# Kernel optimization log

Measured on AMD Instinct MI355X. Metric: run time of the kernel, lower is better.

## Reference

```python
import jax, jax.numpy as jnp
import numpy as np

VOCAB, D_EMB, Z_DIM, HID = 32000, 512, 256, 1024
B, T = 32, 128
PAD_IDX = 0

def setup_inputs() -> dict:
    key = jax.random.key(0)
    ks = jax.random.split(key, 12)
    s_emb = 1.0  # nn.Embedding default N(0,1)
    u = lambda k, shape, fan: jax.random.uniform(k, shape, jnp.float32, -1.0, 1.0) / np.sqrt(fan)
    emb = jax.random.normal(ks[0], (VOCAB, D_EMB), jnp.float32) * s_emb
    emb = emb.at[PAD_IDX].set(0.0)  # padding_idx row zeroed
    inp = {
        "z": jax.random.normal(ks[1], (B, Z_DIM), jnp.float32),
        "x": jax.random.randint(ks[2], (B, T), 0, VOCAB, jnp.int32),
        "W_h": u(ks[3], (HID, Z_DIM), Z_DIM),
        "b_h": u(ks[4], (HID,), Z_DIM),
        "emb": emb,
        "W_ih": u(ks[5], (4 * HID, D_EMB), HID),
        "W_hh": u(ks[6], (4 * HID, HID), HID),
        "b_ih": u(ks[7], (4 * HID,), HID),
        "b_hh": u(ks[8], (4 * HID,), HID),
        "W_out": u(ks[9], (VOCAB, HID), HID),
        "b_out": u(ks[10], (VOCAB,), HID),
    }
    return inp

def _lstm_decode(z, x, W_h, b_h, emb, W_ih, W_hh, b_ih, b_hh, W_out, b_out):
    h0 = jnp.tanh(z @ W_h.T + b_h)            # [B, H]
    c0 = jnp.zeros_like(h0)
    e = emb[x]                                 # [B, T, D]
    # Precompute input-side gate projections for all timesteps at once.
    x_gates = jnp.einsum('btd,gd->btg', e, W_ih) + b_ih + b_hh  # [B, T, 4H]
    x_gates_t = jnp.swapaxes(x_gates, 0, 1)    # [T, B, 4H]

    def step(carry, xg_t):
        h, c = carry
        gates = xg_t + h @ W_hh.T              # [B, 4H]
        i, f, g, o = jnp.split(gates, 4, axis=-1)  # torch gate order i,f,g,o
        i, f, o = jax.nn.sigmoid(i), jax.nn.sigmoid(f), jax.nn.sigmoid(o)
        g = jnp.tanh(g)
        c = f * c + i * g
        h = o * jnp.tanh(c)
        return (h, c), h

    _, hs = jax.lax.scan(step, (h0, c0), x_gates_t)  # hs: [T, B, H]
    out = jnp.swapaxes(hs, 0, 1)               # [B, T, H]
    return jnp.einsum('bth,vh->btv', out, W_out) + b_out  # [B, T, V]

def reference(z, x, W_h, b_h, emb, W_ih, W_hh, b_ih, b_hh, W_out, b_out):
    return _lstm_decode(z, x, W_h, b_h, emb, W_ih, W_hh, b_ih, b_hh, W_out, b_out)
```

## Files before the change

kernel.cpp:

```cpp
#include <hip/hip_runtime.h>

typedef _Float16 f16;
typedef _Float16 f16x8 __attribute__((ext_vector_type(8)));
typedef _Float16 f16x4 __attribute__((ext_vector_type(4)));
typedef float    f32x4 __attribute__((ext_vector_type(4)));
typedef unsigned long long ull;

static constexpr int Bb  = 32;
static constexpr int Tt  = 128;
static constexpr int HID = 1024;
static constexpr int ZD  = 256;
static constexpr int DE  = 512;
static constexpr int VOC = 32000;
static constexpr int BT  = Bb * Tt;
static constexpr int G4  = 4 * HID;
static constexpr int NLSTM = 64;
static constexpr int NTILES = (BT / 256) * (VOC / 256);

__device__ __forceinline__ void gld_lds16(const void* g, void* l) {
  __builtin_amdgcn_global_load_lds((const __attribute__((address_space(1))) unsigned int*)g,
                                   (__attribute__((address_space(3))) unsigned int*)l,
                                   16, 0, 0);
}

__global__ void cvt_kernel(const float* __restrict__ s, f16* __restrict__ d, int n4) {
  int i = blockIdx.x * blockDim.x + threadIdx.x;
  int st = gridDim.x * blockDim.x;
  for (; i < n4; i += st) {
    float4 v = ((const float4*)s)[i];
    f16x4 o = { (f16)v.x, (f16)v.y, (f16)v.z, (f16)v.w };
    ((f16x4*)d)[i] = o;
  }
}

__global__ void gather_kernel(const float* __restrict__ emb, const int* __restrict__ x,
                              f16* __restrict__ E) {
  int g = blockIdx.x * 256 + threadIdx.x;
  int m = g >> 6, seg = (g & 63) * 8;
  int idx = x[m];
  const float* src = emb + (size_t)idx * DE + seg;
  float4 a = *(const float4*)src;
  float4 b = *(const float4*)(src + 4);
  f16x8 o = { (f16)a.x,(f16)a.y,(f16)a.z,(f16)a.w,(f16)b.x,(f16)b.y,(f16)b.z,(f16)b.w };
  *(f16x8*)(E + (size_t)m * DE + seg) = o;
}

__global__ void bsum_kernel(const float* __restrict__ a, const float* __restrict__ b,
                            float* __restrict__ o, int n) {
  int i = blockIdx.x * blockDim.x + threadIdx.x;
  if (i < n) o[i] = a[i] + b[i];
}

__global__ __launch_bounds__(256) void h0_kernel(const float* __restrict__ z,
                                                 const float* __restrict__ W_h,
                                                 const float* __restrict__ b_h,
                                                 f16* __restrict__ h0f) {
  __shared__ float zs[32][260];
  __shared__ float wsl[8][260];
  const int jc = blockIdx.x, tid = threadIdx.x;
  #pragma unroll
  for (int it = 0; it < 8; ++it) {
    int idx = it * 256 + tid;
    float4 v = ((const float4*)z)[idx];
    int b = idx >> 6, k = (idx & 63) * 4;
    zs[b][k] = v.x; zs[b][k+1] = v.y; zs[b][k+2] = v.z; zs[b][k+3] = v.w;
  }
  #pragma unroll
  for (int it = 0; it < 2; ++it) {
    int idx = it * 256 + tid;
    float4 v = ((const float4*)(W_h + (size_t)jc * 8 * ZD))[idx];
    int r = idx >> 6, k = (idx & 63) * 4;
    wsl[r][k] = v.x; wsl[r][k+1] = v.y; wsl[r][k+2] = v.z; wsl[r][k+3] = v.w;
  }
  __syncthreads();
  const int b = tid >> 3, jj = tid & 7;
  const int j = jc * 8 + jj;
  float acc = b_h[j];
  for (int k = 0; k < ZD; ++k) acc += zs[b][k] * wsl[jj][k];
  h0f[(size_t)b * HID + j] = (f16)tanhf(acc);
}

__global__ __launch_bounds__(256, 2) void gemmxg_kernel(
    const f16* __restrict__ A, const f16* __restrict__ B,
    const float* __restrict__ bias, float* __restrict__ C,
    int M, int N, int K) {
  __shared__ f16 As[128 * 64];
  __shared__ f16 Bs[128 * 64];
  const int n0 = blockIdx.x * 128, m0 = blockIdx.y * 128;
  const int tid = threadIdx.x, wid = tid >> 6, lane = tid & 63;
  const int wm = wid >> 1, wn = wid & 1;
  const int sr = lane >> 3, sk = (lane & 7) * 8;
  f32x4 acc[4][4] = {};
  for (int k0 = 0; k0 < K; k0 += 64) {
    __syncthreads();
    #pragma unroll
    for (int i = 0; i < 4; ++i) {
      int rr = (wid * 4 + i) * 8;
      gld_lds16(A + (size_t)(m0 + rr + sr) * K + k0 + sk, &As[rr * 64]);
      gld_lds16(B + (size_t)(n0 + rr + sr) * K + k0 + sk, &Bs[rr * 64]);
    }
    __syncthreads();
    #pragma unroll
    for (int ks = 0; ks < 2; ++ks) {
      f16x8 af[4], bf[4];
      #pragma unroll
      for (int mt = 0; mt < 4; ++mt)
        af[mt] = *(const f16x8*)&As[(wm * 64 + mt * 16 + (lane & 15)) * 64 + ks * 32 + (lane >> 4) * 8];
      #pragma unroll
      for (int nt = 0; nt < 4; ++nt)
        bf[nt] = *(const f16x8*)&Bs[(wn * 64 + nt * 16 + (lane & 15)) * 64 + ks * 32 + (lane >> 4) * 8];
      #pragma unroll
      for (int mt = 0; mt < 4; ++mt)
        #pragma unroll
        for (int nt = 0; nt < 4; ++nt)
          acc[mt][nt] = __builtin_amdgcn_mfma_f32_16x16x32_f16(af[mt], bf[nt], acc[mt][nt], 0, 0, 0);
    }
  }
  #pragma unroll
  for (int nt = 0; nt < 4; ++nt) {
    int col = n0 + wn * 64 + nt * 16 + (lane & 15);
    float bv = bias[col];
    #pragma unroll
    for (int mt = 0; mt < 4; ++mt) {
      int row = m0 + wm * 64 + mt * 16 + (lane >> 4) * 4;
      int b = row >> 7, t0 = row & 127;
      float4 v = { acc[mt][nt][0] + bv, acc[mt][nt][1] + bv,
                   acc[mt][nt][2] + bv, acc[mt][nt][3] + bv };
      *(float4*)&C[((size_t)col * 32 + b) * 128 + t0] = v;
    }
  }
}

static constexpr int SM_HL   = 0;
static constexpr int SM_PART = 66048;
static constexpr int SM_IDX  = 133632;
static constexpr int SM_SIZE = 133648;

__device__ void lstm_role(const f16* __restrict__ Whh16, const float* __restrict__ XG2,
                          const f16* __restrict__ h0f, f16* __restrict__ HS,
                          unsigned* __restrict__ bar, unsigned* __restrict__ gready,
                          char* smem) {
  const int bid = blockIdx.x, tid = threadIdx.x;
  const int lane = tid & 63, wid = tid >> 6;
  const int lr = lane & 15, hi = lane >> 4;
  const int j0 = bid * 16;
  f16 (*hl)[1032] = (f16 (*)[1032])(smem + SM_HL);
  float (*part)[64][33] = (float (*)[64][33])(smem + SM_PART);

  f16x8 wfrag[4][4];
  #pragma unroll
  for (int rt = 0; rt < 4; ++rt) {
    int g = rt * HID + j0 + lr;
    #pragma unroll
    for (int kk = 0; kk < 4; ++kk)
      wfrag[rt][kk] = *(const f16x8*)(Whh16 + (size_t)g * HID + wid * 128 + kk * 32 + hi * 8);
  }

  const int ub = tid & 15, bb = tid >> 4;
  float creg = 0.f;

  for (int t = 0; t < Tt; ++t) {
    float xg[4];
    #pragma unroll
    for (int q = 0; q < 4; ++q)
      xg[q] = XG2[((size_t)(q * HID + j0 + ub) * 32 + bb) * 128 + t];

    if (t > 0) {
      if (wid == 0) {
        const unsigned tgt = (unsigned)t;
        for (;;) {
          unsigned f = __hip_atomic_load(&bar[lane], __ATOMIC_RELAXED, __HIP_MEMORY_SCOPE_AGENT);
          if (__all(f >= tgt)) break;
        }
        if (bid == 0 && lane == 0)
          __hip_atomic_store(gready, (unsigned)t, __ATOMIC_RELAXED, __HIP_MEMORY_SCOPE_AGENT);
      }
      __syncthreads();
    }

    {
      ull tmp[4][4];
      #pragma unroll
      for (int r = 0; r < 4; ++r) {
        int row = wid * 4 + r;
        const f16* hb = (t == 0) ? (h0f + (size_t)row * HID)
                                 : (HS + (size_t)((t - 1) * 32 + row) * HID);
        #pragma unroll
        for (int c = 0; c < 4; ++c)
          tmp[r][c] = ((const ull*)hb)[c * 64 + lane];
      }
      #pragma unroll
      for (int r = 0; r < 4; ++r) {
        int row = wid * 4 + r;
        #pragma unroll
        for (int c = 0; c < 4; ++c)
          *(ull*)&hl[row][(c * 64 + lane) * 4] = tmp[r][c];
      }
    }
    __syncthreads();

    {
      f32x4 acc[4][2] = {};
      #pragma unroll
      for (int kk = 0; kk < 4; ++kk) {
        int ko = wid * 128 + kk * 32 + hi * 8;
        f16x8 bf0 = *(const f16x8*)&hl[lr][ko];
        f16x8 bf1 = *(const f16x8*)&hl[16 + lr][ko];
        #pragma unroll
        for (int rt = 0; rt < 4; ++rt) {
          acc[rt][0] = __builtin_amdgcn_mfma_f32_16x16x32_f16(wfrag[rt][kk], bf0, acc[rt][0], 0, 0, 0);
          acc[rt][1] = __builtin_amdgcn_mfma_f32_16x16x32_f16(wfrag[rt][kk], bf1, acc[rt][1], 0, 0, 0);
        }
      }
      #pragma unroll
      for (int rt = 0; rt < 4; ++rt)
        #pragma unroll
        for (int bt = 0; bt < 2; ++bt)
          #pragma unroll
          for (int p = 0; p < 4; ++p)
            part[wid][rt * 16 + hi * 4 + p][bt * 16 + lr] = acc[rt][bt][p];
    }
    __syncthreads();

    {
      float g4[4];
      #pragma unroll
      for (int q = 0; q < 4; ++q) {
        int i = q * 16 + ub;
        float s = xg[q];
        #pragma unroll
        for (int w = 0; w < 8; ++w) s += part[w][i][bb];
        g4[q] = s;
      }
      float ig = 1.f / (1.f + __expf(-g4[0]));
      float fg = 1.f / (1.f + __expf(-g4[1]));
      float gg = tanhf(g4[2]);
      float og = 1.f / (1.f + __expf(-g4[3]));
      creg = fg * creg + ig * gg;
      float h = og * tanhf(creg);
      union { f16 h; unsigned short u; } cv;
      cv.h = (f16)h;
      __hip_atomic_store((unsigned short*)&HS[(size_t)(t * 32 + bb) * HID + j0 + ub],
                         cv.u, __ATOMIC_RELAXED, __HIP_MEMORY_SCOPE_AGENT);
    }

    asm volatile("s_waitcnt vmcnt(0)" ::: "memory");
    __syncthreads();
    if (tid == 0)
      __hip_atomic_store(&bar[bid], (unsigned)(t + 1),
                         __ATOMIC_RELAXED, __HIP_MEMORY_SCOPE_AGENT);
  }

  if (bid == 0) {
    if (wid == 0) {
      for (;;) {
        unsigned f = __hip_atomic_load(&bar[lane], __ATOMIC_RELAXED, __HIP_MEMORY_SCOPE_AGENT);
        if (__all(f >= (unsigned)Tt)) break;
      }
      if (lane == 0)
        __hip_atomic_store(gready, (unsigned)Tt, __ATOMIC_RELAXED, __HIP_MEMORY_SCOPE_AGENT);
    }
    __syncthreads();
  }
}

__device__ void worker_role(const f16* __restrict__ HS, const f16* __restrict__ Wout16,
                            const float* __restrict__ b_out, float* __restrict__ out,
                            unsigned* __restrict__ gready, unsigned* __restrict__ cnt,
                            char* smem) {
  const int tid = threadIdx.x, wid = tid >> 6, lane = tid & 63;
  const int wm = wid >> 2, wn = wid & 3;
  const int lr = lane & 15, hi = lane >> 4;
  const int srow = lane >> 2;
  const int scol = ((lane & 3) ^ ((lane >> 3) & 3)) * 8;
  const int sx   = (hi ^ ((lr >> 1) & 3)) * 8;
  f16* As = (f16*)(smem);
  f16* Bs = (f16*)(smem + 65536);
  unsigned* sIdx = (unsigned*)(smem + SM_IDX);
  const int cb0 = wid * 2, cb1 = wid * 2 + 1;

  for (;;) {
    if (tid == 0) *sIdx = atomicAdd(cnt, 1u);
    __syncthreads();
    unsigned idx = *sIdx;
    if (idx >= (unsigned)NTILES) break;
    int mg = idx / 125, ng = idx - mg * 125;
    if (wid == 0) {
      const unsigned tgt = (unsigned)(8 * mg + 8);
      for (;;) {
        unsigned g = __hip_atomic_load(gready, __ATOMIC_RELAXED, __HIP_MEMORY_SCOPE_AGENT);
        if (g >= tgt) break;
        __builtin_amdgcn_s_sleep(64);
      }
    }
    __syncthreads();

    const int m0 = mg * 256, n0 = ng * 256;
    f32x4 acc[8][4] = {};

    auto STAGE = [&](int kt) {
      const int k0 = kt << 5, buf = kt & 3;
      gld_lds16(HS     + (size_t)(m0 + cb0 * 16 + srow) * HID + k0 + scol, As + buf * 8192 + cb0 * 512);
      gld_lds16(Wout16 + (size_t)(n0 + cb0 * 16 + srow) * HID + k0 + scol, Bs + buf * 8192 + cb0 * 512);
      gld_lds16(HS     + (size_t)(m0 + cb1 * 16 + srow) * HID + k0 + scol, As + buf * 8192 + cb1 * 512);
      gld_lds16(Wout16 + (size_t)(n0 + cb1 * 16 + srow) * HID + k0 + scol, Bs + buf * 8192 + cb1 * 512);
    };

    STAGE(0); STAGE(1); STAGE(2);
    for (int kt = 0; kt < 32; ++kt) {
      if (kt < 30)       asm volatile("s_waitcnt vmcnt(8)" ::: "memory");
      else if (kt == 30) asm volatile("s_waitcnt vmcnt(4)" ::: "memory");
      else               asm volatile("s_waitcnt vmcnt(0)" ::: "memory");
      __builtin_amdgcn_s_barrier();
      if (kt + 3 < 32) STAGE(kt + 3);
      const f16* as = As + (kt & 3) * 8192;
      const f16* bs = Bs + (kt & 3) * 8192;
      f16x8 af[8], bf[4];
      #pragma unroll
      for (int mt = 0; mt < 8; ++mt)
        af[mt] = *(const f16x8*)&as[(wm * 128 + mt * 16 + lr) * 32 + sx];
      #pragma unroll
      for (int nt = 0; nt < 4; ++nt)
        bf[nt] = *(const f16x8*)&bs[(wn * 64 + nt * 16 + lr) * 32 + sx];
      __builtin_amdgcn_s_setprio(1);
      #pragma unroll
      for (int mt = 0; mt < 8; ++mt)
        #pragma unroll
        for (int nt = 0; nt < 4; ++nt)
          acc[mt][nt] = __builtin_amdgcn_mfma_f32_16x16x32_f16(af[mt], bf[nt], acc[mt][nt], 0, 0, 0);
      __builtin_amdgcn_s_setprio(0);
    }

    #pragma unroll
    for (int nt = 0; nt < 4; ++nt) {
      int col = n0 + wn * 64 + nt * 16 + lr;
      float bv = b_out[col];
      #pragma unroll
      for (int mt = 0; mt < 8; ++mt) {
        int mbase = m0 + wm * 128 + mt * 16 + hi * 4;
        #pragma unroll
        for (int p = 0; p < 4; ++p) {
          int mp = mbase + p;
          int orow = (mp & 31) * 128 + (mp >> 5);
          out[(size_t)orow * VOC + col] = acc[mt][nt][p] + bv;
        }
      }
    }
    __syncthreads();
  }
}

__global__ __launch_bounds__(512, 1) void fused_kernel(
    const f16* __restrict__ Whh16, const float* __restrict__ XG2,
    const f16* __restrict__ h0f, f16* __restrict__ HS,
    const f16* __restrict__ Wout16, const float* __restrict__ b_out,
    float* __restrict__ out, unsigned* __restrict__ bar, unsigned* __restrict__ cnt,
    unsigned* __restrict__ gready) {
  __shared__ __align__(16) char smem[SM_SIZE];
  if (blockIdx.x < NLSTM)
    lstm_role(Whh16, XG2, h0f, HS, bar, gready, smem);
  worker_role(HS, Wout16, b_out, out, gready, cnt, smem);
}

extern "C" void kernel_launch(void* const* d_in, const int* in_sizes, int n_in,
                              void* d_out, int out_size, void* d_ws, size_t ws_size,
                              hipStream_t stream) {
  const float* z     = (const float*)d_in[0];
  const int*   x     = (const int*)d_in[1];
  const float* W_h   = (const float*)d_in[2];
  const float* b_h   = (const float*)d_in[3];
  const float* emb   = (const float*)d_in[4];
  const float* W_ih  = (const float*)d_in[5];
  const float* W_hh  = (const float*)d_in[6];
  const float* b_ih  = (const float*)d_in[7];
  const float* b_hh  = (const float*)d_in[8];
  const float* W_out = (const float*)d_in[9];
  const float* b_out = (const float*)d_in[10];
  float* out = (float*)d_out;

  char* ws = (char*)d_ws;
  size_t off = 0;
  auto carve = [&](size_t n) { char* p = ws + off; off += (n + 255) & ~(size_t)255; return p; };
  f16*   E16    = (f16*)carve((size_t)BT * DE * 2);
  f16*   Wih16  = (f16*)carve((size_t)G4 * DE * 2);
  f16*   Whh16  = (f16*)carve((size_t)G4 * HID * 2);
  f16*   Wout16 = (f16*)carve((size_t)VOC * HID * 2);
  float* XG2    = (float*)carve((size_t)BT * G4 * 4);
  f16*   HS     = (f16*)carve((size_t)BT * HID * 2);
  f16*   h0f    = (f16*)carve((size_t)Bb * HID * 2);
  float* bs     = (float*)carve((size_t)G4 * 4);
  unsigned* bar    = (unsigned*)carve(256);
  unsigned* cnt    = (unsigned*)carve(256);
  unsigned* gready = (unsigned*)carve(256);

  (void)hipMemsetAsync(bar, 0, 768, stream);

  cvt_kernel<<<2048, 256, 0, stream>>>(W_ih,  Wih16,  G4 * DE / 4);
  cvt_kernel<<<2048, 256, 0, stream>>>(W_hh,  Whh16,  G4 * HID / 4);
  cvt_kernel<<<2048, 256, 0, stream>>>(W_out, Wout16, VOC * HID / 4);
  gather_kernel<<<BT * DE / 8 / 256, 256, 0, stream>>>(emb, x, E16);
  bsum_kernel<<<16, 256, 0, stream>>>(b_ih, b_hh, bs, G4);
  h0_kernel<<<128, 256, 0, stream>>>(z, W_h, b_h, h0f);

  dim3 g1(G4 / 128, BT / 128);
  gemmxg_kernel<<<g1, 256, 0, stream>>>(E16, Wih16, bs, XG2, BT, G4, DE);

  fused_kernel<<<256, 512, 0, stream>>>(Whh16, XG2, h0f, HS, Wout16, b_out, out,
                                        bar, cnt, gready);
}
```

Baseline: 933.1 us.

## Replace per-step block barriers with LDS flag polling and per-wave h slices

Wave 0 now mirrors the global per-block progress flags into LDS while it polls them. The other waves spin on their own slice of those LDS flags instead of waiting at a workgroup barrier. The h-state load is repartitioned so each wave fetches only the k-range (its 128 columns) it later consumes in its MFMA. That removes the __syncthreads between the global load and the LDS read. The aim is to cut two block-wide barriers per timestep on the serial LSTM critical path, at the cost of extra LDS spinning and subtler memory-ordering assumptions.

```diff
diff --git a/kernel.cpp b/kernel.cpp
--- a/kernel.cpp
+++ b/kernel.cpp
@@ -133,8 +133,9 @@
 
 static constexpr int SM_HL   = 0;
 static constexpr int SM_PART = 66048;
-static constexpr int SM_IDX  = 133632;
-static constexpr int SM_SIZE = 133648;
+static constexpr int SM_FL   = 133632;
+static constexpr int SM_IDX  = 133888;
+static constexpr int SM_SIZE = 133904;
 
 __device__ void lstm_role(const f16* __restrict__ Whh16, const float* __restrict__ XG2,
                           const f16* __restrict__ h0f, f16* __restrict__ HS,
@@ -146,6 +147,9 @@
   const int j0 = bid * 16;
   f16 (*hl)[1032] = (f16 (*)[1032])(smem + SM_HL);
   float (*part)[64][33] = (float (*)[64][33])(smem + SM_PART);
+  unsigned* fl = (unsigned*)(smem + SM_FL);
+
+  if (tid < 64) fl[tid] = 0;
 
   f16x8 wfrag[4][4];
   #pragma unroll
@@ -158,6 +162,7 @@
 
   const int ub = tid & 15, bb = tid >> 4;
   float creg = 0.f;
+  __syncthreads();
 
   for (int t = 0; t < Tt; ++t) {
     float xg[4];
@@ -167,37 +172,33 @@
 
     if (t > 0) {
       if (wid == 0) {
-        const unsigned tgt = (unsigned)t;
         for (;;) {
           unsigned f = __hip_atomic_load(&bar[lane], __ATOMIC_RELAXED, __HIP_MEMORY_SCOPE_AGENT);
-          if (__all(f >= tgt)) break;
+          __hip_atomic_store(&fl[lane], f, __ATOMIC_RELAXED, __HIP_MEMORY_SCOPE_WORKGROUP);
+          if (__all(f >= (unsigned)t)) break;
         }
         if (bid == 0 && lane == 0)
           __hip_atomic_store(gready, (unsigned)t, __ATOMIC_RELAXED, __HIP_MEMORY_SCOPE_AGENT);
-      }
-      __syncthreads();
+      } else {
+        const int p = wid * 8 + (lane & 7);
+        for (;;) {
+          unsigned f = __hip_atomic_load(&fl[p], __ATOMIC_RELAXED, __HIP_MEMORY_SCOPE_WORKGROUP);
+          if (__all(f >= (unsigned)t)) break;
+        }
+      }
     }
 
     {
-      ull tmp[4][4];
-      #pragma unroll
-      for (int r = 0; r < 4; ++r) {
-        int row = wid * 4 + r;
+      const int uo = wid * 128 + (lane & 31) * 4;
+      #pragma unroll
+      for (int ps = 0; ps < 16; ++ps) {
+        int row = ps * 2 + (lane >> 5);
         const f16* hb = (t == 0) ? (h0f + (size_t)row * HID)
                                  : (HS + (size_t)((t - 1) * 32 + row) * HID);
-        #pragma unroll
-        for (int c = 0; c < 4; ++c)
-          tmp[r][c] = ((const ull*)hb)[c * 64 + lane];
-      }
-      #pragma unroll
-      for (int r = 0; r < 4; ++r) {
-        int row = wid * 4 + r;
-        #pragma unroll
-        for (int c = 0; c < 4; ++c)
-          *(ull*)&hl[row][(c * 64 + lane) * 4] = tmp[r][c];
-      }
-    }
-    __syncthreads();
+        ull v = *(const ull*)(hb + uo);
+        *(ull*)&hl[row][uo] = v;
+      }
+    }
 
     {
       f32x4 acc[4][2] = {};
```

Result: faster. 907.5 us (-2.8%).
